# Performance work log

Measured on AMD Instinct MI355X. Metric: run time of the kernel, lower is better.

Reference implementation:

```python
import jax, jax.numpy as jnp
import numpy as np

N_FEATURES = 256
HIDDEN_DIM = 256
NUM_HEADS = 8
HEAD_DIM = HIDDEN_DIM // NUM_HEADS
SCALE = HEAD_DIM ** -0.5
H = W = 64


def setup_inputs() -> dict:
    key = jax.random.key(0)
    k1, k2, kq, kk, kv, kp, kb = jax.random.split(key, 7)
    s = 1.0 / np.sqrt(N_FEATURES)
    return {
        "x1": jax.random.normal(k1, (1, N_FEATURES, H, W), dtype=jnp.float32),
        "x2": jax.random.normal(k2, (1, N_FEATURES, H, W), dtype=jnp.float32),
        # 1x1 conv weights reduce to [out_ch, in_ch] matrices
        "Wq": jax.random.uniform(kq, (HIDDEN_DIM, N_FEATURES), jnp.float32, -s, s),
        "Wk": jax.random.uniform(kk, (HIDDEN_DIM, N_FEATURES), jnp.float32, -s, s),
        "Wv": jax.random.uniform(kv, (HIDDEN_DIM, N_FEATURES), jnp.float32, -s, s),
        "Wp": jax.random.uniform(kp, (N_FEATURES, HIDDEN_DIM), jnp.float32, -s, s),
        "bp": jax.random.uniform(kb, (N_FEATURES,), jnp.float32, -s, s),
    }


def reference(x1, x2, Wq, Wk, Wv, Wp, bp):
    B, C, Hh, Ww = x1.shape
    N = Hh * Ww
    # 1x1 convs == channel matmuls; reshape to [B, heads, head_dim, N]
    q = jnp.einsum('oc,bchw->bohw', Wq, x1).reshape(B, NUM_HEADS, HEAD_DIM, N)
    k = jnp.einsum('oc,bchw->bohw', Wk, x2).reshape(B, NUM_HEADS, HEAD_DIM, N)
    v = jnp.einsum('oc,bchw->bohw', Wv, x2).reshape(B, NUM_HEADS, HEAD_DIM, N)
    attn = jnp.einsum('bhcn,bhcm->bhnm', q, k) * SCALE
    attn = jax.nn.softmax(attn, axis=-1)
    fused = jnp.einsum('bhnm,bhcm->bhcn', attn, v)
    fused = fused.reshape(B, HIDDEN_DIM, Hh, Ww)  # requires hidden_dim == C
    out = jnp.einsum('oc,bchw->bohw', Wp, fused) + bp[None, :, None, None]
    return out
```

## Files before the change

### kernel.cpp

```cpp
#include <hip/hip_runtime.h>

#define NPOS 4096
#define NCH  256
#define HD   32
#define KB   128
#define NSPLIT 4
#define SPLIT_KEYS (NPOS / NSPLIT)
#define NSTEP (SPLIT_KEYS / KB)

#define TOFF(o, c) (((((o) >> 4) * 8 + ((c) >> 5)) * 64 + \
                     ((((c) >> 3) & 3) * 16) + ((o) & 15)) * 8 + ((c) & 7))

typedef float f32x4  __attribute__((ext_vector_type(4)));
typedef float f32x16 __attribute__((ext_vector_type(16)));
typedef short s16x8  __attribute__((ext_vector_type(8)));
typedef uint  u32x2  __attribute__((ext_vector_type(2)));
typedef uint  u32x4  __attribute__((ext_vector_type(4)));
typedef int   i32x2  __attribute__((ext_vector_type(2)));

static __device__ __forceinline__ s16x8 load8(const ushort* p) {
    return *(const s16x8*)p;
}
static __device__ __forceinline__ ushort bfbits(float x) {
    __bf16 b = (__bf16)x;
    return __builtin_bit_cast(unsigned short, b);
}
static __device__ __forceinline__ float bfval(ushort u) {
    uint x = (uint)u << 16;
    return __builtin_bit_cast(float, x);
}
static __device__ __forceinline__ uint pk2(float a, float b) {
    return (uint)bfbits(a) | ((uint)bfbits(b) << 16);
}
static __device__ __forceinline__ void plswap(uint& a, uint& b) {
    i32x2 r = __builtin_amdgcn_permlane32_swap((int)a, (int)b, false, false);
    a = (uint)r[0];
    b = (uint)r[1];
}

__global__ __launch_bounds__(256) void convert_kernel(
    const float* __restrict__ x1, const float* __restrict__ x2,
    const float* __restrict__ Wq, const float* __restrict__ Wk,
    const float* __restrict__ Wv, const float* __restrict__ Wp,
    ushort* __restrict__ xt1h, ushort* __restrict__ xt1l,
    ushort* __restrict__ xt2h, ushort* __restrict__ xt2l,
    ushort* __restrict__ wsp, float qscale)
{
    if (blockIdx.z == 2) {
        const int m = blockIdx.y;
        const float* src = m == 0 ? Wq : m == 1 ? Wk : m == 2 ? Wv : Wp;
        const float sc = m == 0 ? qscale : 1.f;
        const int idx = (blockIdx.x * 256 + threadIdx.x) * 4;
        const int o = idx >> 8, c0 = idx & 255;
        f32x4 w = *(const f32x4*)(src + idx);
        w *= sc;
        ushort h[4], l[4];
#pragma unroll
        for (int i = 0; i < 4; ++i) {
            h[i] = bfbits(w[i]);
            l[i] = bfbits(w[i] - bfval(h[i]));
        }
        ushort* H = wsp + m * 2 * 65536;
        const int off = TOFF(o, c0);
        *(u32x2*)(H + off)         = (u32x2){(uint)h[0] | ((uint)h[1] << 16),
                                             (uint)h[2] | ((uint)h[3] << 16)};
        *(u32x2*)(H + 65536 + off) = (u32x2){(uint)l[0] | ((uint)l[1] << 16),
                                             (uint)l[2] | ((uint)l[3] << 16)};
        return;
    }
    __shared__ float tile[64][65];
    const float* X = blockIdx.z ? x2 : x1;
    ushort* Hd = blockIdx.z ? xt2h : xt1h;
    ushort* Ld = blockIdx.z ? xt2l : xt1l;
    const int n0 = blockIdx.x * 64, c0 = blockIdx.y * 64;
    const int tj = threadIdx.x & 63, ti = threadIdx.x >> 6;
#pragma unroll
    for (int r = 0; r < 16; ++r) {
        int i = r * 4 + ti;
        tile[i][tj] = X[(c0 + i) * NPOS + n0 + tj];
    }
    __syncthreads();
#pragma unroll
    for (int r = 0; r < 16; ++r) {
        int i = r * 4 + ti;
        float v = tile[tj][i];
        ushort h = bfbits(v);
        ushort l = bfbits(v - bfval(h));
        const int off = TOFF(n0 + i, c0 + tj);
        Hd[off] = h;
        Ld[off] = l;
    }
}

__global__ __launch_bounds__(256) void gemm_qkv_kernel(
    const ushort* __restrict__ wsp,
    const ushort* __restrict__ x1h, const ushort* __restrict__ x1l,
    const ushort* __restrict__ x2h, const ushort* __restrict__ x2l,
    ushort* __restrict__ qt, ushort* __restrict__ kt, ushort* __restrict__ vt)
{
    const int m  = blockIdx.y >> 2;
    const int ob = blockIdx.y & 3;
    const ushort* Wh = wsp + m * 131072;
    const ushort* Wl = Wh + 65536;
    const ushort* Bh = (m == 0) ? x1h : x2h;
    const ushort* Bl = (m == 0) ? x1l : x2l;

    const int wid = threadIdx.x >> 6, lane = threadIdx.x & 63;
    const int lq = lane & 15, grp = lane >> 4;
    const int o0 = ob * 64 + wid * 16;
    const int n0 = blockIdx.x * 32;
    const int To = o0 >> 4;
    const int Tn = n0 >> 4;

    f32x4 acc[2];
    acc[0] = (f32x4){0.f, 0.f, 0.f, 0.f};
    acc[1] = acc[0];
#pragma unroll
    for (int kc = 0; kc < 8; ++kc) {
        const s16x8 ah = load8(Wh + ((To * 8 + kc) * 64 + lane) * 8);
        const s16x8 al = load8(Wl + ((To * 8 + kc) * 64 + lane) * 8);
#pragma unroll
        for (int nt = 0; nt < 2; ++nt) {
            const s16x8 bh = load8(Bh + (((Tn + nt) * 8 + kc) * 64 + lane) * 8);
            const s16x8 bl = load8(Bl + (((Tn + nt) * 8 + kc) * 64 + lane) * 8);
            acc[nt] = __builtin_amdgcn_mfma_f32_16x16x32_bf16(ah, bh, acc[nt], 0, 0, 0);
            acc[nt] = __builtin_amdgcn_mfma_f32_16x16x32_bf16(ah, bl, acc[nt], 0, 0, 0);
            acc[nt] = __builtin_amdgcn_mfma_f32_16x16x32_bf16(al, bh, acc[nt], 0, 0, 0);
        }
    }
    if (m < 2) {
        ushort* Y = m ? kt : qt;
        const int head = o0 >> 5, d0 = (o0 & 31) + grp * 4;
#pragma unroll
        for (int nt = 0; nt < 2; ++nt) {
            const int n = n0 + nt * 16 + lq;
            *(u32x2*)(Y + head * (NPOS * HD) + n * HD + d0) =
                (u32x2){pk2(acc[nt][0], acc[nt][1]), pk2(acc[nt][2], acc[nt][3])};
        }
    } else {
#pragma unroll
        for (int nt = 0; nt < 2; ++nt) {
            const int n = n0 + nt * 16 + lq;
#pragma unroll
            for (int r = 0; r < 4; ++r)
                vt[(o0 + grp * 4 + r) * NPOS + n] = bfbits(acc[nt][r]);
        }
    }
}

__global__ __launch_bounds__(256) void attn_mfma_kernel(
    const ushort* __restrict__ Qt,
    const ushort* __restrict__ Kt,
    const ushort* __restrict__ Vt,
    ushort* __restrict__ Opb,
    float* __restrict__ Ml)
{
    __shared__ __align__(16) ushort lds[18944];
    const int bid  = blockIdx.x;
    const int s    = bid >> 8;
    const int h    = bid & 7;
    const int qblk = (bid & 255) >> 3;
    const int tid  = threadIdx.x;
    const int wid  = tid >> 6;
    const int lane = tid & 63;
    const int l31  = lane & 31;
    const int hi   = lane >> 5;
    const int q0   = qblk * 128 + wid * 32;
    const int k0   = s * SPLIT_KEYS;
    const int hq   = h * (NPOS * HD);

    s16x8 qf[2];
#pragma unroll
    for (int kh = 0; kh < 2; ++kh)
        qf[kh] = load8(Qt + hq + (q0 + l31) * HD + kh * 16 + hi * 8);

    const int kr0 = tid >> 2, kc0 = tid & 3;
    const ushort* kS = Kt + hq + kr0 * HD + kc0 * 8;
    const int kdst0 = kr0 * 40 + ((kc0 ^ ((kr0 >> 3) & 3)) & 3) * 8;
    const int kdst1 = kdst0 + 64 * 40;

    const int vr0 = tid >> 4, vc0 = tid & 15;
    const ushort* vS = Vt + h * (HD * NPOS) + vr0 * NPOS + vc0 * 8;
    const int vdst0 = vr0 * 136 + ((vc0 ^ ((vr0 >> 3) & 3)) & 15) * 8;
    const int vdst1 = (vr0 + 16) * 136 +
                      ((vc0 ^ (((vr0 + 16) >> 3) & 3)) & 15) * 8;

    const int kx = l31 >> 3;

    s16x8 onesf;
#pragma unroll
    for (int i = 0; i < 8; ++i) onesf[i] = (short)0x3F80;

    f32x16 oacc = {};
    f32x16 accl = {};

    *(s16x8*)(lds + kdst0)         = load8(kS + (size_t)k0 * HD);
    *(s16x8*)(lds + kdst1)         = load8(kS + (size_t)k0 * HD + 64 * HD);
    *(s16x8*)(lds + 10240 + vdst0) = load8(vS + k0);
    *(s16x8*)(lds + 10240 + vdst1) = load8(vS + k0 + 16 * NPOS);
    int m1 = (NSTEP > 1) ? k0 + KB : k0;
    s16x8 kra = load8(kS + (size_t)m1 * HD);
    s16x8 krb = load8(kS + (size_t)m1 * HD + 64 * HD);
    s16x8 vra = load8(vS + m1);
    s16x8 vrb = load8(vS + m1 + 16 * NPOS);
    __syncthreads();

    for (int step = 0; step < NSTEP; ++step) {
        const int cur = step & 1;
        ushort* const Kb = lds + cur * 5120;
        ushort* const Vb = lds + 10240 + cur * 4352;

        {
            ushort* const Kn = lds + (cur ^ 1) * 5120;
            ushort* const Vn = lds + 10240 + (cur ^ 1) * 4352;
            *(s16x8*)(Kn + kdst0) = kra;
            *(s16x8*)(Kn + kdst1) = krb;
            *(s16x8*)(Vn + vdst0) = vra;
            *(s16x8*)(Vn + vdst1) = vrb;
        }
        const int mn = (step + 2 < NSTEP) ? k0 + (step + 2) * KB : k0;
        kra = load8(kS + (size_t)mn * HD);
        krb = load8(kS + (size_t)mn * HD + 64 * HD);
        vra = load8(vS + mn);
        vrb = load8(vS + mn + 16 * NPOS);

#pragma unroll
        for (int t = 0; t < 4; ++t) {
            const int krow = (t * 32 + l31) * 40;
            const s16x8 kfa = *(const s16x8*)(Kb + krow + ((hi ^ kx) & 3) * 8);
            const s16x8 kfb = *(const s16x8*)(Kb + krow + (((2 + hi) ^ kx) & 3) * 8);
            f32x16 st = {};
            __builtin_amdgcn_s_setprio(1);
            st = __builtin_amdgcn_mfma_f32_32x32x16_bf16(kfa, qf[0], st, 0, 0, 0);
            st = __builtin_amdgcn_mfma_f32_32x32x16_bf16(kfb, qf[1], st, 0, 0, 0);
            __builtin_amdgcn_s_setprio(0);

            const s16x8 vf0 = *(const s16x8*)(Vb + l31 * 136 +
                                              (((t * 4 + hi) ^ kx) & 15) * 8);
            const s16x8 vf1 = *(const s16x8*)(Vb + l31 * 136 +
                                              (((t * 4 + 2 + hi) ^ kx) & 15) * 8);

            uint w[4], w2[4];
#pragma unroll
            for (int g = 0; g < 4; ++g) {
                const float p0 = __builtin_amdgcn_exp2f(st[4 * g + 0]);
                const float p1 = __builtin_amdgcn_exp2f(st[4 * g + 1]);
                const float p2 = __builtin_amdgcn_exp2f(st[4 * g + 2]);
                const float p3 = __builtin_amdgcn_exp2f(st[4 * g + 3]);
                w[g]  = pk2(p0, p1);
                w2[g] = pk2(p2, p3);
            }
            uint a0 = w[0],  c0 = w[1];  plswap(a0, c0);
            uint a1 = w2[0], c1 = w2[1]; plswap(a1, c1);
            const s16x8 pfA = __builtin_bit_cast(s16x8, (u32x4){a0, a1, c0, c1});
            uint b0 = w[2],  d0 = w[3];  plswap(b0, d0);
            uint b1 = w2[2], d1 = w2[3]; plswap(b1, d1);
            const s16x8 pfB = __builtin_bit_cast(s16x8, (u32x4){b0, b1, d0, d1});

            __builtin_amdgcn_s_setprio(1);
            oacc = __builtin_amdgcn_mfma_f32_32x32x16_bf16(vf0, pfA, oacc, 0, 0, 0);
            oacc = __builtin_amdgcn_mfma_f32_32x32x16_bf16(vf1, pfB, oacc, 0, 0, 0);
            accl = __builtin_amdgcn_mfma_f32_32x32x16_bf16(onesf, pfA, accl, 0, 0, 0);
            accl = __builtin_amdgcn_mfma_f32_32x32x16_bf16(onesf, pfB, accl, 0, 0, 0);
            __builtin_amdgcn_s_setprio(0);
        }

        __syncthreads();
    }

    const int n = q0 + l31;
    ushort* Ops = Opb + (size_t)s * (NPOS * NCH) + n * NCH + h * HD;
#pragma unroll
    for (int g = 0; g < 4; ++g) {
        *(u32x2*)(Ops + g * 8 + hi * 4) =
            (u32x2){pk2(oacc[4 * g + 0], oacc[4 * g + 1]),
                    pk2(oacc[4 * g + 2], oacc[4 * g + 3])};
    }
    if (lane < 32)
        Ml[(s * 8 + h) * NPOS + n] = accl[0];
}

__global__ __launch_bounds__(256) void combine_kernel(
    const ushort* __restrict__ Opb, const float* __restrict__ Ml,
    ushort* __restrict__ FH, ushort* __restrict__ FL)
{
    const int n = blockIdx.x * 4 + (threadIdx.x >> 6);
    const int c = (threadIdx.x & 63) * 4;
    const int h = c >> 5;
    float l = 0.f;
#pragma unroll
    for (int s = 0; s < NSPLIT; ++s)
        l += Ml[(s * 8 + h) * NPOS + n];
    const float inv = 1.f / l;

    float sum[4] = {0.f, 0.f, 0.f, 0.f};
#pragma unroll
    for (int s = 0; s < NSPLIT; ++s) {
        const u32x2 raw = *(const u32x2*)(Opb + (size_t)s * (NPOS * NCH) +
                                          n * NCH + c);
        sum[0] += bfval((ushort)(raw[0] & 0xFFFF));
        sum[1] += bfval((ushort)(raw[0] >> 16));
        sum[2] += bfval((ushort)(raw[1] & 0xFFFF));
        sum[3] += bfval((ushort)(raw[1] >> 16));
    }
    ushort hb[4], lb[4];
#pragma unroll
    for (int i = 0; i < 4; ++i) {
        float f = sum[i] * inv;
        hb[i] = bfbits(f);
        lb[i] = bfbits(f - bfval(hb[i]));
    }
    const int off = TOFF(n, c);
    *(u32x2*)(FH + off) = (u32x2){(uint)hb[0] | ((uint)hb[1] << 16),
                                  (uint)hb[2] | ((uint)hb[3] << 16)};
    *(u32x2*)(FL + off) = (u32x2){(uint)lb[0] | ((uint)lb[1] << 16),
                                  (uint)lb[2] | ((uint)lb[3] << 16)};
}

__global__ __launch_bounds__(256) void gemm_out_kernel(
    const ushort* __restrict__ Wh, const ushort* __restrict__ Wl,
    const ushort* __restrict__ Bh, const ushort* __restrict__ Bl,
    const float* __restrict__ bias, float* __restrict__ Y)
{
    const int wid = threadIdx.x >> 6, lane = threadIdx.x & 63;
    const int lq = lane & 15, grp = lane >> 4;
    const int o0 = blockIdx.y * 64 + wid * 16;
    const int n0 = blockIdx.x * 32;
    const int To = o0 >> 4;
    const int Tn = n0 >> 4;

    f32x4 acc[2];
    acc[0] = (f32x4){0.f, 0.f, 0.f, 0.f};
    acc[1] = acc[0];
#pragma unroll
    for (int kc = 0; kc < 8; ++kc) {
        const s16x8 ah = load8(Wh + ((To * 8 + kc) * 64 + lane) * 8);
        const s16x8 al = load8(Wl + ((To * 8 + kc) * 64 + lane) * 8);
#pragma unroll
        for (int nt = 0; nt < 2; ++nt) {
            const s16x8 bh = load8(Bh + (((Tn + nt) * 8 + kc) * 64 + lane) * 8);
            const s16x8 bl = load8(Bl + (((Tn + nt) * 8 + kc) * 64 + lane) * 8);
            acc[nt] = __builtin_amdgcn_mfma_f32_16x16x32_bf16(ah, bh, acc[nt], 0, 0, 0);
            acc[nt] = __builtin_amdgcn_mfma_f32_16x16x32_bf16(ah, bl, acc[nt], 0, 0, 0);
            acc[nt] = __builtin_amdgcn_mfma_f32_16x16x32_bf16(al, bh, acc[nt], 0, 0, 0);
        }
    }
    const f32x4 b4 = *(const f32x4*)(bias + o0 + grp * 4);
#pragma unroll
    for (int nt = 0; nt < 2; ++nt) {
        const int n = n0 + nt * 16 + lq;
#pragma unroll
        for (int r = 0; r < 4; ++r)
            Y[(o0 + grp * 4 + r) * NPOS + n] = acc[nt][r] + b4[r];
    }
}

extern "C" void kernel_launch(void* const* d_in, const int* in_sizes, int n_in,
                              void* d_out, int out_size, void* d_ws, size_t ws_size,
                              hipStream_t stream) {
    const float* x1 = (const float*)d_in[0];
    const float* x2 = (const float*)d_in[1];
    const float* Wq = (const float*)d_in[2];
    const float* Wk = (const float*)d_in[3];
    const float* Wv = (const float*)d_in[4];
    const float* Wp = (const float*)d_in[5];
    const float* bp = (const float*)d_in[6];
    float* out = (float*)d_out;

    const size_t MB = 1u << 20;
    char* wsc = (char*)d_ws;
    ushort* xt1h = (ushort*)(wsc + 0 * MB);
    ushort* xt1l = (ushort*)(wsc + 2 * MB);
    ushort* xt2h = (ushort*)(wsc + 4 * MB);
    ushort* xt2l = (ushort*)(wsc + 6 * MB);
    ushort* qt   = (ushort*)(wsc + 8 * MB);
    ushort* kt   = (ushort*)(wsc + 10 * MB);
    ushort* vt   = (ushort*)(wsc + 12 * MB);
    ushort* wsp  = (ushort*)(wsc + 14 * MB);
    float*  Ml   = (float*)(wsc + 15 * MB);
    ushort* Opb  = (ushort*)(wsc + 0 * MB);
    ushort* fth  = (ushort*)(wsc + 8 * MB);
    ushort* ftl  = (ushort*)(wsc + 10 * MB);

    const float qscale = (float)(0.17677669529663687 * 1.4426950408889634);

    convert_kernel<<<dim3(64, 4, 3), 256, 0, stream>>>(
        x1, x2, Wq, Wk, Wv, Wp, xt1h, xt1l, xt2h, xt2l, wsp, qscale);

    gemm_qkv_kernel<<<dim3(128, 12), 256, 0, stream>>>(
        wsp, xt1h, xt1l, xt2h, xt2l, qt, kt, vt);

    attn_mfma_kernel<<<1024, 256, 0, stream>>>(qt, kt, vt, Opb, Ml);

    combine_kernel<<<1024, 256, 0, stream>>>(Opb, Ml, fth, ftl);

    ushort* wph = wsp + 393216;
    ushort* wpl = wsp + 458752;
    gemm_out_kernel<<<dim3(128, 4), 256, 0, stream>>>(
        wph, wpl, fth, ftl, bp, out);
}
```

Baseline: 75.58 us.

## Halve attention key tile, compute row sums on VALU, raise occupancy

Halves the key/value tile per pipeline step, which shrinks LDS per block and lets the kernel request 8 blocks per CU through launch bounds. The softmax denominator, previously obtained with two extra MFMAs against a ones matrix, is now accumulated in fp32 VALU adds and finished with a cross-half lane swap. The intent is to cut MFMA work by a third, free the accumulator registers, and improve latency hiding through higher occupancy. In exchange there are twice as many barrier-synchronised steps, and the row sum now comes from unrounded fp32 probabilities instead of the bf16 values used in P·V.

Result: slower. 84.96 us (+12.4%).

```diff
diff --git a/kernel.cpp b/kernel.cpp
--- a/kernel.cpp
+++ b/kernel.cpp
@@ -3,7 +3,7 @@
 #define NPOS 4096
 #define NCH  256
 #define HD   32
-#define KB   128
+#define KB   64
 #define NSPLIT 4
 #define SPLIT_KEYS (NPOS / NSPLIT)
 #define NSTEP (SPLIT_KEYS / KB)
@@ -148,14 +148,14 @@
     }
 }
 
-__global__ __launch_bounds__(256) void attn_mfma_kernel(
+__global__ __launch_bounds__(256, 8) void attn_mfma_kernel(
     const ushort* __restrict__ Qt,
     const ushort* __restrict__ Kt,
     const ushort* __restrict__ Vt,
     ushort* __restrict__ Opb,
     float* __restrict__ Ml)
 {
-    __shared__ __align__(16) ushort lds[18944];
+    __shared__ __align__(16) ushort lds[9728];
     const int bid  = blockIdx.x;
     const int s    = bid >> 8;
     const int h    = bid & 7;
@@ -176,80 +176,68 @@
 
     const int kr0 = tid >> 2, kc0 = tid & 3;
     const ushort* kS = Kt + hq + kr0 * HD + kc0 * 8;
-    const int kdst0 = kr0 * 40 + ((kc0 ^ ((kr0 >> 3) & 3)) & 3) * 8;
-    const int kdst1 = kdst0 + 64 * 40;
-
-    const int vr0 = tid >> 4, vc0 = tid & 15;
+    const int kdst = kr0 * 40 + (((kc0 ^ (kr0 >> 3)) & 3) << 3);
+
+    const int vr0 = tid >> 3, vc0 = tid & 7;
     const ushort* vS = Vt + h * (HD * NPOS) + vr0 * NPOS + vc0 * 8;
-    const int vdst0 = vr0 * 136 + ((vc0 ^ ((vr0 >> 3) & 3)) & 15) * 8;
-    const int vdst1 = (vr0 + 16) * 136 +
-                      ((vc0 ^ (((vr0 + 16) >> 3) & 3)) & 15) * 8;
+    const int vdst = vr0 * 72 + (((vc0 ^ (vr0 >> 3)) & 7) << 3);
 
     const int kx = l31 >> 3;
 
-    s16x8 onesf;
-#pragma unroll
-    for (int i = 0; i < 8; ++i) onesf[i] = (short)0x3F80;
-
     f32x16 oacc = {};
-    f32x16 accl = {};
-
-    *(s16x8*)(lds + kdst0)         = load8(kS + (size_t)k0 * HD);
-    *(s16x8*)(lds + kdst1)         = load8(kS + (size_t)k0 * HD + 64 * HD);
-    *(s16x8*)(lds + 10240 + vdst0) = load8(vS + k0);
-    *(s16x8*)(lds + 10240 + vdst1) = load8(vS + k0 + 16 * NPOS);
-    int m1 = (NSTEP > 1) ? k0 + KB : k0;
+    float lacc = 0.f;
+
+    *(s16x8*)(lds + kdst)        = load8(kS + (size_t)k0 * HD);
+    *(s16x8*)(lds + 5120 + vdst) = load8(vS + k0);
+    const int m1 = (NSTEP > 1) ? k0 + KB : k0;
     s16x8 kra = load8(kS + (size_t)m1 * HD);
-    s16x8 krb = load8(kS + (size_t)m1 * HD + 64 * HD);
     s16x8 vra = load8(vS + m1);
-    s16x8 vrb = load8(vS + m1 + 16 * NPOS);
     __syncthreads();
 
     for (int step = 0; step < NSTEP; ++step) {
         const int cur = step & 1;
-        ushort* const Kb = lds + cur * 5120;
-        ushort* const Vb = lds + 10240 + cur * 4352;
+        ushort* const Kb = lds + cur * 2560;
+        ushort* const Vb = lds + 5120 + cur * 2304;
 
         {
-            ushort* const Kn = lds + (cur ^ 1) * 5120;
-            ushort* const Vn = lds + 10240 + (cur ^ 1) * 4352;
-            *(s16x8*)(Kn + kdst0) = kra;
-            *(s16x8*)(Kn + kdst1) = krb;
-            *(s16x8*)(Vn + vdst0) = vra;
-            *(s16x8*)(Vn + vdst1) = vrb;
+            ushort* const Kn = lds + (cur ^ 1) * 2560;
+            ushort* const Vn = lds + 5120 + (cur ^ 1) * 2304;
+            *(s16x8*)(Kn + kdst) = kra;
+            *(s16x8*)(Vn + vdst) = vra;
         }
         const int mn = (step + 2 < NSTEP) ? k0 + (step + 2) * KB : k0;
         kra = load8(kS + (size_t)mn * HD);
-        krb = load8(kS + (size_t)mn * HD + 64 * HD);
         vra = load8(vS + mn);
-        vrb = load8(vS + mn + 16 * NPOS);
-
-#pragma unroll
-        for (int t = 0; t < 4; ++t) {
+
+#pragma unroll
+        for (int t = 0; t < 2; ++t) {
             const int krow = (t * 32 + l31) * 40;
-            const s16x8 kfa = *(const s16x8*)(Kb + krow + ((hi ^ kx) & 3) * 8);
-            const s16x8 kfb = *(const s16x8*)(Kb + krow + (((2 + hi) ^ kx) & 3) * 8);
+            const s16x8 kfa = *(const s16x8*)(Kb + krow + (((hi ^ kx) & 3) << 3));
+            const s16x8 kfb = *(const s16x8*)(Kb + krow + ((((2 + hi) ^ kx) & 3) << 3));
             f32x16 st = {};
             __builtin_amdgcn_s_setprio(1);
             st = __builtin_amdgcn_mfma_f32_32x32x16_bf16(kfa, qf[0], st, 0, 0, 0);
             st = __builtin_amdgcn_mfma_f32_32x32x16_bf16(kfb, qf[1], st, 0, 0, 0);
             __builtin_amdgcn_s_setprio(0);
 
-            const s16x8 vf0 = *(const s16x8*)(Vb + l31 * 136 +
-                                              (((t * 4 + hi) ^ kx) & 15) * 8);
-            const s16x8 vf1 = *(const s16x8*)(Vb + l31 * 136 +
-                                              (((t * 4 + 2 + hi) ^ kx) & 15) * 8);
+            const s16x8 vf0 = *(const s16x8*)(Vb + l31 * 72 +
+                                              ((((t * 4 + hi) ^ kx) & 7) << 3));
+            const s16x8 vf1 = *(const s16x8*)(Vb + l31 * 72 +
+                                              ((((t * 4 + 2 + hi) ^ kx) & 7) << 3));
 
             uint w[4], w2[4];
+            float ls = 0.f;
 #pragma unroll
             for (int g = 0; g < 4; ++g) {
                 const float p0 = __builtin_amdgcn_exp2f(st[4 * g + 0]);
                 const float p1 = __builtin_amdgcn_exp2f(st[4 * g + 1]);
                 const float p2 = __builtin_amdgcn_exp2f(st[4 * g + 2]);
                 const float p3 = __builtin_amdgcn_exp2f(st[4 * g + 3]);
+                ls += (p0 + p1) + (p2 + p3);
                 w[g]  = pk2(p0, p1);
                 w2[g] = pk2(p2, p3);
             }
+            lacc += ls;
             uint a0 = w[0],  c0 = w[1];  plswap(a0, c0);
             uint a1 = w2[0], c1 = w2[1]; plswap(a1, c1);
             const s16x8 pfA = __builtin_bit_cast(s16x8, (u32x4){a0, a1, c0, c1});
@@ -260,12 +248,16 @@
             __builtin_amdgcn_s_setprio(1);
             oacc = __builtin_amdgcn_mfma_f32_32x32x16_bf16(vf0, pfA, oacc, 0, 0, 0);
             oacc = __builtin_amdgcn_mfma_f32_32x32x16_bf16(vf1, pfB, oacc, 0, 0, 0);
-            accl = __builtin_amdgcn_mfma_f32_32x32x16_bf16(onesf, pfA, accl, 0, 0, 0);
-            accl = __builtin_amdgcn_mfma_f32_32x32x16_bf16(onesf, pfB, accl, 0, 0, 0);
             __builtin_amdgcn_s_setprio(0);
         }
 
         __syncthreads();
+    }
+
+    {
+        uint a = __builtin_bit_cast(uint, lacc), b = a;
+        plswap(a, b);
+        lacc = __builtin_bit_cast(float, a) + __builtin_bit_cast(float, b);
     }
 
     const int n = q0 + l31;
@@ -277,7 +269,7 @@
                     pk2(oacc[4 * g + 2], oacc[4 * g + 3])};
     }
     if (lane < 32)
-        Ml[(s * 8 + h) * NPOS + n] = accl[0];
+        Ml[(s * 8 + h) * NPOS + n] = lacc;
 }
 
 __global__ __launch_bounds__(256) void combine_kernel(
```
